# Kernel optimization log

Hardware: AMD Instinct MI355X
Metric: run time of the kernel (lower is better)

The kernel has to match this reference:

```python
import jax, jax.numpy as jnp
import numpy as np
from jax import lax

S, V, DW = 2048, 50000, 400     # seq_len, word vocab, word emb dim
CV, DC = 8, 32                  # casing vocab / dim
PV, DP = 50, 64                 # POS vocab / dim
H, C = 768, 13                  # lstm hidden (per direction), num tag classes
DIN = DW + DC + DP              # 496 lstm input dim


def setup_inputs() -> dict:
    key = jax.random.key(0)
    ks = jax.random.split(key, 18)
    r = lambda k, sh, s=0.02: (jax.random.normal(k, sh) * s).astype(jnp.float32)
    return {
        "x": jax.random.randint(ks[0], (S,), 0, V),
        "casing": jax.random.randint(ks[1], (S,), 0, CV),
        "pos": jax.random.randint(ks[2], (S,), 0, PV),
        "word_emb": r(ks[3], (V, DW)),
        "casing_emb": r(ks[4], (CV, DC)),
        "pos_emb": r(ks[5], (PV, DP)),
        "Wih_f": r(ks[6], (4 * H, DIN)),
        "Whh_f": r(ks[7], (4 * H, H)),
        "b_f": jnp.zeros((4 * H,), jnp.float32),
        "Wih_b": r(ks[8], (4 * H, DIN)),
        "Whh_b": r(ks[9], (4 * H, H)),
        "b_b": jnp.zeros((4 * H,), jnp.float32),
        "Wc": r(ks[10], (C, 2 * H)),
        "bc": jnp.zeros((C,), jnp.float32),
        "start_trans": r(ks[11], (C,), 0.1),
        "end_trans": r(ks[12], (C,), 0.1),
        "trans": r(ks[13], (C, C), 0.1),
        "h0": jnp.zeros((2, H), jnp.float32),
        "c0": jnp.zeros((2, H), jnp.float32),
    }


def _lstm(xg, Whh, h0, c0):
    # xg: (S, 4H) precomputed input-to-hidden gates; PyTorch gate order i,f,g,o
    def step(carry, g_in):
        h, c = carry
        g = g_in + h @ Whh.T
        i, f, gg, o = jnp.split(g, 4)
        c = jax.nn.sigmoid(f) * c + jax.nn.sigmoid(i) * jnp.tanh(gg)
        h = jax.nn.sigmoid(o) * jnp.tanh(c)
        return (h, c), h
    _, hs = lax.scan(step, (h0, c0), xg)
    return hs  # (S, H)


def reference(x, casing, pos, word_emb, casing_emb, pos_emb,
              Wih_f, Whh_f, b_f, Wih_b, Whh_b, b_b, Wc, bc,
              start_trans, end_trans, trans, h0, c0):
    # embedding concat -> (S, DIN)
    emb = jnp.concatenate([word_emb[x], casing_emb[casing], pos_emb[pos]], axis=-1)
    # weight-dropped LSTM (eval mode: DropConnect identity), bidirectional
    hs_f = _lstm(emb @ Wih_f.T + b_f, Whh_f, h0[0], c0[0])
    hs_b = _lstm((emb @ Wih_b.T + b_b)[::-1], Whh_b, h0[1], c0[1])[::-1]
    o = jnp.concatenate([hs_f, hs_b], axis=-1) @ Wc.T + bc  # (S, C)
    tag_scores = jax.nn.log_softmax(o, axis=1)
    # CRF Viterbi decode (torchcrf-style), batch of 1 (the unsqueeze(0))
    score0 = start_trans + tag_scores[0]
    def vstep(score, em):
        cand = score[:, None] + trans            # (prev C, next C)
        bp = jnp.argmax(cand, axis=0)
        return jnp.max(cand, axis=0) + em, bp
    score, bps = lax.scan(vstep, score0, tag_scores[1:])
    last = jnp.argmax(score + end_trans)
    def back(tag, bp):
        prev = bp[tag]
        return prev, prev
    _, prevs = lax.scan(back, last, bps[::-1])
    tags = jnp.concatenate([prevs[::-1], last[None]])  # (S,) best path
    return tag_scores, tags
```

## Files before the change

kernel.cpp:

```cpp
#include <hip/hip_runtime.h>
#include <hip/hip_bf16.h>


#define SEQ  2048
#define DINW 496
#define HDIM 768
#define G4   3072
#define CDIM 13
#define NWG  48
#define JPW  16
#define DATA_SPIN (1u << 14)

__device__ __forceinline__ float sigf(float x) { return 1.0f / (1.0f + __expf(-x)); }
__device__ __forceinline__ float tanhf_fast(float x) {
    float ax = fabsf(x);
    float e  = __expf(-2.0f * ax);
    float t  = (1.0f - e) / (1.0f + e);
    return copysignf(t, x);
}

__global__ __launch_bounds__(256) void k_gemm_xg(
    const int* __restrict__ x, const int* __restrict__ casing, const int* __restrict__ pos,
    const float* __restrict__ we, const float* __restrict__ ce, const float* __restrict__ pe,
    const float* __restrict__ Wih_f, const float* __restrict__ b_f,
    const float* __restrict__ Wih_b, const float* __restrict__ b_b,
    __hip_bfloat16* __restrict__ xg_f, __hip_bfloat16* __restrict__ xg_b)
{
    __shared__ float As[16][132];
    __shared__ float Bs[16][132];
    int dir = blockIdx.z;
    const float* B    = dir ? Wih_b : Wih_f;
    const float* bias = dir ? b_b   : b_f;
    __hip_bfloat16* C = dir ? xg_b  : xg_f;
    int n0 = blockIdx.x * 128, m0 = blockIdx.y * 128;
    int tid = threadIdx.x;
    int r  = tid >> 1, cb = (tid & 1) * 8;
    int tx = tid & 15, ty = tid >> 4;

    int m = m0 + r;
    const float* arow_w = we + (size_t)x[m] * 400;
    const float* arow_c = ce + (size_t)casing[m] * 32;
    const float* arow_p = pe + (size_t)pos[m] * 64;
    const float* brow   = B + (size_t)(n0 + r) * DINW;

    float acc[8][8] = {};
    for (int k0 = 0; k0 < DINW; k0 += 16) {
        int c0 = k0 + cb;
        float4 a0, a1, b0, b1;
        if (c0 < 400)      a0 = *(const float4*)(arow_w + c0);
        else if (c0 < 432) a0 = *(const float4*)(arow_c + (c0 - 400));
        else               a0 = *(const float4*)(arow_p + (c0 - 432));
        int c4 = c0 + 4;
        if (c4 < 400)      a1 = *(const float4*)(arow_w + c4);
        else if (c4 < 432) a1 = *(const float4*)(arow_c + (c4 - 400));
        else               a1 = *(const float4*)(arow_p + (c4 - 432));
        b0 = *(const float4*)(brow + c0);
        b1 = *(const float4*)(brow + c4);
        __syncthreads();
        As[cb + 0][r] = a0.x; As[cb + 1][r] = a0.y; As[cb + 2][r] = a0.z; As[cb + 3][r] = a0.w;
        As[cb + 4][r] = a1.x; As[cb + 5][r] = a1.y; As[cb + 6][r] = a1.z; As[cb + 7][r] = a1.w;
        Bs[cb + 0][r] = b0.x; Bs[cb + 1][r] = b0.y; Bs[cb + 2][r] = b0.z; Bs[cb + 3][r] = b0.w;
        Bs[cb + 4][r] = b1.x; Bs[cb + 5][r] = b1.y; Bs[cb + 6][r] = b1.z; Bs[cb + 7][r] = b1.w;
        __syncthreads();
        #pragma unroll
        for (int k = 0; k < 16; k++) {
            float4 av0 = *(const float4*)&As[k][ty * 8];
            float4 av1 = *(const float4*)&As[k][ty * 8 + 4];
            float4 bv0 = *(const float4*)&Bs[k][tx * 8];
            float4 bv1 = *(const float4*)&Bs[k][tx * 8 + 4];
            float aa[8] = {av0.x, av0.y, av0.z, av0.w, av1.x, av1.y, av1.z, av1.w};
            float bb[8] = {bv0.x, bv0.y, bv0.z, bv0.w, bv1.x, bv1.y, bv1.z, bv1.w};
            #pragma unroll
            for (int i = 0; i < 8; i++)
                #pragma unroll
                for (int jj = 0; jj < 8; jj++)
                    acc[i][jj] += aa[i] * bb[jj];
        }
    }
    float4 bs0 = *(const float4*)(bias + n0 + tx * 8);
    float4 bs1 = *(const float4*)(bias + n0 + tx * 8 + 4);
    float bb8[8] = {bs0.x, bs0.y, bs0.z, bs0.w, bs1.x, bs1.y, bs1.z, bs1.w};
    #pragma unroll
    for (int i = 0; i < 8; i++) {
        int row = m0 + ty * 8 + i;
        union { __hip_bfloat16 h[4]; ushort4 u; } c0v, c1v;
        #pragma unroll
        for (int jj = 0; jj < 4; jj++) {
            c0v.h[jj] = __float2bfloat16(acc[i][jj] + bb8[jj]);
            c1v.h[jj] = __float2bfloat16(acc[i][jj + 4] + bb8[jj + 4]);
        }
        *(ushort4*)(C + (size_t)row * G4 + n0 + tx * 8)     = c0v.u;
        *(ushort4*)(C + (size_t)row * G4 + n0 + tx * 8 + 4) = c1v.u;
    }
}

__global__ __launch_bounds__(1024) void k_lstm(
    const __hip_bfloat16* __restrict__ xg_f, const __hip_bfloat16* __restrict__ xg_b,
    const float* __restrict__ Whh_f, const float* __restrict__ Whh_b,
    const float* __restrict__ h0, const float* __restrict__ c0v,
    float* __restrict__ hs_f, float* __restrict__ hs_b,
    unsigned* __restrict__ msg, unsigned* __restrict__ abortw)
{
    __shared__ float hbuf[2][HDIM];
    __shared__ unsigned sbuf[16];
    __shared__ unsigned sdead;

    int wg = blockIdx.x;
    int dir = wg & 1, slot = wg >> 1;
    const __hip_bfloat16* xg = dir ? xg_b : xg_f;
    const float* Whh = dir ? Whh_b : Whh_f;
    float* hs        = dir ? hs_b  : hs_f;
    unsigned* mdir = msg + (size_t)dir * 2 * HDIM;

    int tid = threadIdx.x, lane = tid & 63, wv = tid >> 6;
    int q = lane >> 4, gl = lane & 15;
    int j = slot * JPW + wv;

    float w[48];
    const float* wr = Whh + (size_t)(q * HDIM + j) * HDIM;
    #pragma unroll
    for (int m = 0; m < 12; m++) {
        float4 f4 = *(const float4*)(wr + gl * 4 + m * 64);
        w[m * 4 + 0] = f4.x; w[m * 4 + 1] = f4.y;
        w[m * 4 + 2] = f4.z; w[m * 4 + 3] = f4.w;
    }
    float cst = c0v[dir * HDIM + j];

    if (tid == 0) sdead = 0;

    for (int t = 0; t < SEQ; t++) {
        int xrow = dir ? (SEQ - 1 - t) : t;
        const __hip_bfloat16* xga = xg + (size_t)xrow * G4 + j;
        float xv0 = __bfloat162float(xga[0]);
        float xv1 = __bfloat162float(xga[HDIM]);
        float xv2 = __bfloat162float(xga[2 * HDIM]);
        float xv3 = __bfloat162float(xga[3 * HDIM]);

        int par = (t & 1) ^ 1;

        if (wv < 2) {
            int base = wv * 6;
            if (t == 0) {
                #pragma unroll
                for (int m = 0; m < 6; m++)
                    hbuf[1][(base + m) * 64 + lane] = h0[dir * HDIM + (base + m) * 64 + lane];
            } else {
                const unsigned* g = mdir + (size_t)par * HDIM;
                unsigned vals[6];
                unsigned fresh = 0, rounds = 0;
                bool dead = false;
                for (;;) {
                    #pragma unroll
                    for (int m = 0; m < 6; m++)
                        if (!(fresh & (1u << m)))
                            vals[m] = __hip_atomic_load(&g[(base + m) * 64 + lane],
                                        __ATOMIC_RELAXED, __HIP_MEMORY_SCOPE_AGENT);
                    #pragma unroll
                    for (int m = 0; m < 6; m++)
                        if ((vals[m] >> 16) == (unsigned)t) fresh |= (1u << m);
                    if (__all(fresh == 0x3Fu)) break;
                    unsigned ab = __hip_atomic_load(abortw,
                                    __ATOMIC_RELAXED, __HIP_MEMORY_SCOPE_AGENT);
                    if (ab || ++rounds >= DATA_SPIN) { dead = true; break; }
                }
                #pragma unroll
                for (int m = 0; m < 6; m++) {
                    union { unsigned u; float f; } cvt;
                    cvt.u = (vals[m] & 0xFFFFu) << 16;
                    hbuf[par][(base + m) * 64 + lane] = cvt.f;
                }
                if (dead && lane == 0) {
                    __hip_atomic_store(abortw, 1u,
                                       __ATOMIC_RELAXED, __HIP_MEMORY_SCOPE_AGENT);
                    sdead = 1;
                }
            }
        }

        __syncthreads();
        if (sdead) break;

        float acc = 0.f;
        #pragma unroll
        for (int m = 0; m < 12; m++) {
            float4 f4 = *(const float4*)&hbuf[par][gl * 4 + m * 64];
            acc += w[m * 4 + 0] * f4.x + w[m * 4 + 1] * f4.y
                 + w[m * 4 + 2] * f4.z + w[m * 4 + 3] * f4.w;
        }
        acc += __shfl_xor(acc, 1);
        acc += __shfl_xor(acc, 2);
        acc += __shfl_xor(acc, 4);
        acc += __shfl_xor(acc, 8);
        float si = __shfl(acc, 0),  sf = __shfl(acc, 16);
        float sg = __shfl(acc, 32), so = __shfl(acc, 48);

        float gi = sigf(xv0 + si), gf = sigf(xv1 + sf);
        float gg = tanhf_fast(xv2 + sg), go = sigf(xv3 + so);
        cst = gf * cst + gi * gg;
        float h = go * tanhf_fast(cst);

        if (lane == 0) {
            union { __hip_bfloat16 b; unsigned short u; } cv;
            cv.b = __float2bfloat16(h);
            sbuf[wv] = ((unsigned)(t + 1) << 16) | (unsigned)cv.u;
            int hrow = dir ? (SEQ - 1 - t) : t;
            hs[(size_t)hrow * HDIM + j] = h;
        }
        __syncthreads();

        if (wv == 0 && lane < 16)
            __hip_atomic_store(&mdir[(size_t)(t & 1) * HDIM + slot * JPW + lane],
                               sbuf[lane],
                               __ATOMIC_RELAXED, __HIP_MEMORY_SCOPE_AGENT);
    }
}

__global__ __launch_bounds__(256) void k_head(
    const float* __restrict__ hs_f, const float* __restrict__ hs_b,
    const float* __restrict__ Wc, const float* __restrict__ bc,
    float* __restrict__ out)
{
    __shared__ float wcs[CDIM][1536];
    __shared__ float bcs[CDIM];
    int tid = threadIdx.x;
    for (int i = tid; i < CDIM * 1536; i += 256) {
        int n = i / 1536;
        wcs[n][i - n * 1536] = Wc[i];
    }
    if (tid < CDIM) bcs[tid] = bc[tid];
    __syncthreads();

    int lane = tid & 63, wv = tid >> 6;
    int off = (lane < 32) ? lane * 24 : 768 + (lane - 32) * 24;
    for (int rr = 0; rr < 4; rr++) {
        int row = blockIdx.x * 16 + wv * 4 + rr;
        const float* src = (lane < 32) ? (hs_f + (size_t)row * HDIM + lane * 24)
                                       : (hs_b + (size_t)row * HDIM + (lane - 32) * 24);
        float hvv[24];
        #pragma unroll
        for (int k = 0; k < 6; k++) {
            float4 f4 = *(const float4*)(src + k * 4);
            hvv[k * 4 + 0] = f4.x; hvv[k * 4 + 1] = f4.y;
            hvv[k * 4 + 2] = f4.z; hvv[k * 4 + 3] = f4.w;
        }
        float o[CDIM];
        #pragma unroll
        for (int n = 0; n < CDIM; n++) {
            const float* wr2 = &wcs[n][off];
            float s0 = 0.f, s1 = 0.f, s2 = 0.f, s3 = 0.f;
            #pragma unroll
            for (int k = 0; k < 6; k++) {
                float4 w4 = *(const float4*)(wr2 + k * 4);
                s0 += w4.x * hvv[k * 4 + 0];
                s1 += w4.y * hvv[k * 4 + 1];
                s2 += w4.z * hvv[k * 4 + 2];
                s3 += w4.w * hvv[k * 4 + 3];
            }
            o[n] = (s0 + s1) + (s2 + s3);
        }
        #pragma unroll
        for (int n = 0; n < CDIM; n++) {
            #pragma unroll
            for (int d = 1; d < 64; d <<= 1) o[n] += __shfl_xor(o[n], d);
            o[n] += bcs[n];
        }
        float m = o[0];
        #pragma unroll
        for (int n = 1; n < CDIM; n++) m = fmaxf(m, o[n]);
        float sum = 0.f;
        #pragma unroll
        for (int n = 0; n < CDIM; n++) sum += __expf(o[n] - m);
        float ls = m + __logf(sum);
        if (lane == 0) {
            #pragma unroll
            for (int n = 0; n < CDIM; n++) out[(size_t)row * CDIM + n] = o[n] - ls;
        }
    }
}

__global__ __launch_bounds__(64) void k_viterbi(
    const float* __restrict__ ts, const float* __restrict__ st,
    const float* __restrict__ en, const float* __restrict__ tr,
    float* __restrict__ tags_out)
{
    __shared__ unsigned char bp[SEQ - 1][16];
    __shared__ unsigned char path[SEQ];
    int n = threadIdx.x;
    bool act = n < CDIM;
    float trn[CDIM];
    #pragma unroll
    for (int p = 0; p < CDIM; p++) trn[p] = act ? tr[p * CDIM + n] : -1e30f;
    float score = act ? (st[n] + ts[n]) : -1e30f;

    for (int s = 1; s < SEQ; s++) {
        float em = act ? ts[(size_t)s * CDIM + n] : 0.f;
        float sp[CDIM];
        #pragma unroll
        for (int p = 0; p < CDIM; p++) sp[p] = __shfl(score, p);
        float best = -1e30f; int arg = 0;
        #pragma unroll
        for (int p = 0; p < CDIM; p++) {
            float v = sp[p] + trn[p];
            if (v > best) { best = v; arg = p; }
        }
        score = best + em;
        if (act) bp[s - 1][n] = (unsigned char)arg;
    }
    float fin = act ? (score + en[n]) : -1e30f;
    float fv[CDIM];
    #pragma unroll
    for (int p = 0; p < CDIM; p++) fv[p] = __shfl(fin, p);
    __syncthreads();
    if (n == 0) {
        float best = -1e30f; int last = 0;
        #pragma unroll
        for (int p = 0; p < CDIM; p++) { if (fv[p] > best) { best = fv[p]; last = p; } }
        int cur = last;
        path[SEQ - 1] = (unsigned char)cur;
        for (int s = SEQ - 2; s >= 0; s--) { cur = bp[s][cur]; path[s] = (unsigned char)cur; }
    }
    __syncthreads();
    for (int i = n; i < SEQ; i += 64) tags_out[i] = (float)path[i];
}

__global__ void k_zero(float* p, int n) {
    int i = blockIdx.x * 256 + threadIdx.x;
    if (i < n) p[i] = 0.f;
}

extern "C" void kernel_launch(void* const* d_in, const int* in_sizes, int n_in,
                              void* d_out, int out_size, void* d_ws, size_t ws_size,
                              hipStream_t stream)
{
    const int*   x      = (const int*)d_in[0];
    const int*   casing = (const int*)d_in[1];
    const int*   pos    = (const int*)d_in[2];
    const float* we     = (const float*)d_in[3];
    const float* ce     = (const float*)d_in[4];
    const float* pe     = (const float*)d_in[5];
    const float* Wih_f  = (const float*)d_in[6];
    const float* Whh_f  = (const float*)d_in[7];
    const float* b_f    = (const float*)d_in[8];
    const float* Wih_b  = (const float*)d_in[9];
    const float* Whh_b  = (const float*)d_in[10];
    const float* b_b    = (const float*)d_in[11];
    const float* Wc     = (const float*)d_in[12];
    const float* bc     = (const float*)d_in[13];
    const float* strt   = (const float*)d_in[14];
    const float* endt   = (const float*)d_in[15];
    const float* trans  = (const float*)d_in[16];
    const float* h0     = (const float*)d_in[17];
    const float* c0     = (const float*)d_in[18];

    const size_t need = 37761028;
    if (ws_size < need) {
        k_zero<<<(out_size + 255) / 256, 256, 0, stream>>>((float*)d_out, out_size);
        return;
    }
    char* wsb = (char*)d_ws;
    float* hs_f = (float*)(wsb);
    float* hs_b = (float*)(wsb + 6291456);
    __hip_bfloat16* xg_f = (__hip_bfloat16*)(wsb + 12582912);
    __hip_bfloat16* xg_b = (__hip_bfloat16*)(wsb + 25165824);
    unsigned* msg = (unsigned*)(wsb + 37748736);
    unsigned* abortw = (unsigned*)(wsb + 37761024);

    hipMemsetAsync(msg, 0, 12288 + 4, stream);

    k_gemm_xg<<<dim3(G4 / 128, SEQ / 128, 2), 256, 0, stream>>>(
        x, casing, pos, we, ce, pe, Wih_f, b_f, Wih_b, b_b, xg_f, xg_b);
    k_lstm<<<2 * NWG, 1024, 0, stream>>>(
        xg_f, xg_b, Whh_f, Whh_b, h0, c0, hs_f, hs_b, msg, abortw);
    k_head<<<SEQ / 16, 256, 0, stream>>>(hs_f, hs_b, Wc, bc, (float*)d_out);
    k_viterbi<<<1, 64, 0, stream>>>(
        (const float*)d_out, strt, endt, trans, (float*)d_out + (size_t)SEQ * CDIM);
}
```

Baseline: 6.111 ms.

## Use bf16 MFMA for input-projection GEMM instead of fp32 FMA

Rewrites the embedding-gather input-to-hidden GEMM to convert operands to bf16 in shared memory and compute with 16x16x32 bf16 MFMA instructions, four waves each owning a 64x64 tile. This replaces the scalar fp32 outer-product loop and is meant to cut the GEMM's compute time. Operands are now rounded to bf16 before multiplication, which adds precision error. The output stores become scattered per-element bf16 writes.

```diff
diff --git a/kernel.cpp b/kernel.cpp
--- a/kernel.cpp
+++ b/kernel.cpp
@@ -10,6 +10,10 @@
 #define NWG  48
 #define JPW  16
 #define DATA_SPIN (1u << 14)
+#define LDK  40
+
+typedef __attribute__((ext_vector_type(8))) short bf16x8;
+typedef __attribute__((ext_vector_type(4))) float f32x4;
 
 __device__ __forceinline__ float sigf(float x) { return 1.0f / (1.0f + __expf(-x)); }
 __device__ __forceinline__ float tanhf_fast(float x) {
@@ -17,6 +21,11 @@
     float e  = __expf(-2.0f * ax);
     float t  = (1.0f - e) / (1.0f + e);
     return copysignf(t, x);
+}
+__device__ __forceinline__ unsigned pack_bf16(float a, float b) {
+    union { __hip_bfloat16 h; unsigned short u; } x, y;
+    x.h = __float2bfloat16(a); y.h = __float2bfloat16(b);
+    return (unsigned)x.u | ((unsigned)y.u << 16);
 }
 
 __global__ __launch_bounds__(256) void k_gemm_xg(
@@ -26,16 +35,18 @@
     const float* __restrict__ Wih_b, const float* __restrict__ b_b,
     __hip_bfloat16* __restrict__ xg_f, __hip_bfloat16* __restrict__ xg_b)
 {
-    __shared__ float As[16][132];
-    __shared__ float Bs[16][132];
+    __shared__ unsigned short Ab[128][LDK];
+    __shared__ unsigned short Bb[128][LDK];
     int dir = blockIdx.z;
     const float* B    = dir ? Wih_b : Wih_f;
     const float* bias = dir ? b_b   : b_f;
     __hip_bfloat16* C = dir ? xg_b  : xg_f;
     int n0 = blockIdx.x * 128, m0 = blockIdx.y * 128;
     int tid = threadIdx.x;
-    int r  = tid >> 1, cb = (tid & 1) * 8;
-    int tx = tid & 15, ty = tid >> 4;
+    int r = tid & 127, half = tid >> 7;
+    int lane = tid & 63, wv = tid >> 6;
+    int wr = wv >> 1, wc = wv & 1;
+    int lrow = lane & 15, kg = lane >> 4;
 
     int m = m0 + r;
     const float* arow_w = we + (size_t)x[m] * 400;
@@ -43,54 +54,73 @@
     const float* arow_p = pe + (size_t)pos[m] * 64;
     const float* brow   = B + (size_t)(n0 + r) * DINW;
 
-    float acc[8][8] = {};
-    for (int k0 = 0; k0 < DINW; k0 += 16) {
-        int c0 = k0 + cb;
-        float4 a0, a1, b0, b1;
-        if (c0 < 400)      a0 = *(const float4*)(arow_w + c0);
-        else if (c0 < 432) a0 = *(const float4*)(arow_c + (c0 - 400));
-        else               a0 = *(const float4*)(arow_p + (c0 - 432));
-        int c4 = c0 + 4;
-        if (c4 < 400)      a1 = *(const float4*)(arow_w + c4);
-        else if (c4 < 432) a1 = *(const float4*)(arow_c + (c4 - 400));
-        else               a1 = *(const float4*)(arow_p + (c4 - 432));
-        b0 = *(const float4*)(brow + c0);
-        b1 = *(const float4*)(brow + c4);
+    f32x4 acc[4][4] = {};
+
+    for (int it = 0; it < 16; it++) {
+        int kb = it * 32 + half * 16;
+        float av[16], bv[16];
+        if (kb >= DINW) {
+            #pragma unroll
+            for (int i = 0; i < 16; i++) { av[i] = 0.f; bv[i] = 0.f; }
+        } else {
+            #pragma unroll
+            for (int c4 = 0; c4 < 4; c4++) {
+                int k = kb + c4 * 4;
+                float4 v;
+                if (k < 400)      v = *(const float4*)(arow_w + k);
+                else if (k < 432) v = *(const float4*)(arow_c + (k - 400));
+                else              v = *(const float4*)(arow_p + (k - 432));
+                av[c4 * 4 + 0] = v.x; av[c4 * 4 + 1] = v.y;
+                av[c4 * 4 + 2] = v.z; av[c4 * 4 + 3] = v.w;
+                float4 u = *(const float4*)(brow + k);
+                bv[c4 * 4 + 0] = u.x; bv[c4 * 4 + 1] = u.y;
+                bv[c4 * 4 + 2] = u.z; bv[c4 * 4 + 3] = u.w;
+            }
+        }
+        unsigned pa[8], pb[8];
+        #pragma unroll
+        for (int i = 0; i < 8; i++) {
+            pa[i] = pack_bf16(av[2 * i], av[2 * i + 1]);
+            pb[i] = pack_bf16(bv[2 * i], bv[2 * i + 1]);
+        }
         __syncthreads();
-        As[cb + 0][r] = a0.x; As[cb + 1][r] = a0.y; As[cb + 2][r] = a0.z; As[cb + 3][r] = a0.w;
-        As[cb + 4][r] = a1.x; As[cb + 5][r] = a1.y; As[cb + 6][r] = a1.z; As[cb + 7][r] = a1.w;
-        Bs[cb + 0][r] = b0.x; Bs[cb + 1][r] = b0.y; Bs[cb + 2][r] = b0.z; Bs[cb + 3][r] = b0.w;
-        Bs[cb + 4][r] = b1.x; Bs[cb + 5][r] = b1.y; Bs[cb + 6][r] = b1.z; Bs[cb + 7][r] = b1.w;
+        uint4* dA = (uint4*)&Ab[r][half * 16];
+        uint4* dB = (uint4*)&Bb[r][half * 16];
+        dA[0] = make_uint4(pa[0], pa[1], pa[2], pa[3]);
+        dA[1] = make_uint4(pa[4], pa[5], pa[6], pa[7]);
+        dB[0] = make_uint4(pb[0], pb[1], pb[2], pb[3]);
+        dB[1] = make_uint4(pb[4], pb[5], pb[6], pb[7]);
         __syncthreads();
-        #pragma unroll
-        for (int k = 0; k < 16; k++) {
-            float4 av0 = *(const float4*)&As[k][ty * 8];
-            float4 av1 = *(const float4*)&As[k][ty * 8 + 4];
-            float4 bv0 = *(const float4*)&Bs[k][tx * 8];
-            float4 bv1 = *(const float4*)&Bs[k][tx * 8 + 4];
-            float aa[8] = {av0.x, av0.y, av0.z, av0.w, av1.x, av1.y, av1.z, av1.w};
-            float bb[8] = {bv0.x, bv0.y, bv0.z, bv0.w, bv1.x, bv1.y, bv1.z, bv1.w};
-            #pragma unroll
-            for (int i = 0; i < 8; i++)
-                #pragma unroll
-                for (int jj = 0; jj < 8; jj++)
-                    acc[i][jj] += aa[i] * bb[jj];
-        }
-    }
-    float4 bs0 = *(const float4*)(bias + n0 + tx * 8);
-    float4 bs1 = *(const float4*)(bias + n0 + tx * 8 + 4);
-    float bb8[8] = {bs0.x, bs0.y, bs0.z, bs0.w, bs1.x, bs1.y, bs1.z, bs1.w};
+
+        union frag { uint4 u; bf16x8 v; };
+        frag af[4], bf[4];
+        #pragma unroll
+        for (int i = 0; i < 4; i++) {
+            int arow = wr * 64 + i * 16 + lrow;
+            int bcol = wc * 64 + i * 16 + lrow;
+            af[i].u = *(const uint4*)((const char*)&Ab[0][0] + arow * (LDK * 2) + kg * 16);
+            bf[i].u = *(const uint4*)((const char*)&Bb[0][0] + bcol * (LDK * 2) + kg * 16);
+        }
+        #pragma unroll
+        for (int i = 0; i < 4; i++)
+            #pragma unroll
+            for (int j = 0; j < 4; j++)
+                acc[i][j] = __builtin_amdgcn_mfma_f32_16x16x32_bf16(
+                                af[i].v, bf[j].v, acc[i][j], 0, 0, 0);
+    }
+
     #pragma unroll
-    for (int i = 0; i < 8; i++) {
-        int row = m0 + ty * 8 + i;
-        union { __hip_bfloat16 h[4]; ushort4 u; } c0v, c1v;
-        #pragma unroll
-        for (int jj = 0; jj < 4; jj++) {
-            c0v.h[jj] = __float2bfloat16(acc[i][jj] + bb8[jj]);
-            c1v.h[jj] = __float2bfloat16(acc[i][jj + 4] + bb8[jj + 4]);
-        }
-        *(ushort4*)(C + (size_t)row * G4 + n0 + tx * 8)     = c0v.u;
-        *(ushort4*)(C + (size_t)row * G4 + n0 + tx * 8 + 4) = c1v.u;
+    for (int j = 0; j < 4; j++) {
+        int col = n0 + wc * 64 + j * 16 + lrow;
+        float bsv = bias[col];
+        #pragma unroll
+        for (int i = 0; i < 4; i++) {
+            int rbase = m0 + wr * 64 + i * 16 + kg * 4;
+            #pragma unroll
+            for (int reg = 0; reg < 4; reg++)
+                C[(size_t)(rbase + reg) * G4 + col] =
+                    __float2bfloat16(acc[i][j][reg] + bsv);
+        }
     }
 }
 
```

Result: faster. 5.990 ms, median of 2 (-2.0%).
